# Kernel optimization log

Measured on AMD Instinct MI355X. Metric: run time of the kernel, lower is better.

Reference implementation:

```python
import jax, jax.numpy as jnp
import numpy as np

B, N, D, S, H = 32, 4096, 256, 16, 512
ITERS = 3
EPS = 1e-8
LN_EPS = 1e-5  # torch LayerNorm default


def _ln(x, w, b):
    m = jnp.mean(x, axis=-1, keepdims=True)
    v = jnp.mean(jnp.square(x - m), axis=-1, keepdims=True)
    return (x - m) / jnp.sqrt(v + LN_EPS) * w + b


def setup_inputs() -> dict:
    key = jax.random.key(0)
    ks = jax.random.split(key, 20)
    s = 1.0 / np.sqrt(D)
    return {
        "inputs": jax.random.normal(ks[0], (B, N, D), jnp.float32),
        "token_weight": jax.random.uniform(ks[1], (B, N), jnp.float32),
        "noise": jax.random.normal(ks[2], (B, S, D), jnp.float32),
        "ln_in_w": jnp.ones((D,), jnp.float32), "ln_in_b": jnp.zeros((D,), jnp.float32),
        "ln_s_w": jnp.ones((D,), jnp.float32), "ln_s_b": jnp.zeros((D,), jnp.float32),
        "ln_m_w": jnp.ones((D,), jnp.float32), "ln_m_b": jnp.zeros((D,), jnp.float32),
        "Wk": jax.random.normal(ks[3], (D, D), jnp.float32) * s,
        "Wv": jax.random.normal(ks[4], (D, D), jnp.float32) * s,
        "Wq": jax.random.normal(ks[5], (D, D), jnp.float32) * s,
        "gru_wih": jax.random.normal(ks[6], (3 * D, D), jnp.float32) * s,
        "gru_whh": jax.random.normal(ks[7], (3 * D, D), jnp.float32) * s,
        "gru_bih": jax.random.normal(ks[8], (3 * D,), jnp.float32) * s,
        "gru_bhh": jax.random.normal(ks[9], (3 * D,), jnp.float32) * s,
        "mlp_w1": jax.random.normal(ks[10], (H, D), jnp.float32) * s,
        "mlp_b1": jnp.zeros((H,), jnp.float32),
        "mlp_w2": jax.random.normal(ks[11], (D, H), jnp.float32) * (1.0 / np.sqrt(H)),
        "mlp_b2": jnp.zeros((D,), jnp.float32),
        "slots_mu": jax.random.normal(ks[12], (1, 1, D), jnp.float32) * 0.02,
        "slots_logsigma": jax.random.normal(ks[13], (1, 1, D), jnp.float32) * 0.02,
    }


def _gru(x, h, wih, whh, bih, bhh):
    # torch GRUCell: gates ordered r, z, n
    gi = x @ wih.T + bih  # [BS, 3D]
    gh = h @ whh.T + bhh
    ir, iz, inn = jnp.split(gi, 3, axis=-1)
    hr, hz, hn = jnp.split(gh, 3, axis=-1)
    r = jax.nn.sigmoid(ir + hr)
    z = jax.nn.sigmoid(iz + hz)
    n = jnp.tanh(inn + r * hn)
    return (1.0 - z) * n + z * h


def reference(inputs, token_weight, noise, ln_in_w, ln_in_b, ln_s_w, ln_s_b,
              ln_m_w, ln_m_b, Wk, Wv, Wq, gru_wih, gru_whh, gru_bih, gru_bhh,
              mlp_w1, mlp_b1, mlp_w2, mlp_b2, slots_mu, slots_logsigma):
    tw = jnp.clip(token_weight, 0.0, None)  # [B,N]
    x = _ln(inputs, ln_in_w, ln_in_b)
    k = x @ Wk.T  # [B,N,D]
    v = x @ Wv.T
    sigma = jnp.clip(jnp.exp(slots_logsigma), 1e-6, None)
    slots = slots_mu + sigma * noise  # [B,S,D]
    scale = D ** (-0.5)
    attn = None
    for _ in range(ITERS):
        slots_prev = slots
        q = _ln(slots, ln_s_w, ln_s_b) @ Wq.T  # [B,S,D]
        logits = jnp.einsum('bnd,bmd->bnm', k, q) * scale  # [B,N,S]
        attn = jax.nn.softmax(logits, axis=-1)  # softmax over slots
        attn = attn * tw[:, :, None]
        attn = attn / (jnp.sum(attn, axis=1, keepdims=True) + EPS)  # normalize over tokens
        updates = jnp.einsum('bnm,bnd->bmd', attn, v)  # [B,S,D]
        slots = _gru(updates.reshape(B * S, D), slots_prev.reshape(B * S, D),
                     gru_wih, gru_whh, gru_bih, gru_bhh).reshape(B, S, D)
        h = jax.nn.gelu(_ln(slots, ln_m_w, ln_m_b) @ mlp_w1.T + mlp_b1, approximate=False)
        slots = slots + h @ mlp_w2.T + mlp_b2
    return slots, attn
```

## Files before the change

### kernel.cpp

```cpp
#include <hip/hip_runtime.h>
#include <hip/hip_bf16.h>
#include <math.h>


#define EPS_ 1e-8f
#define LNEPS_ 1e-5f

typedef __attribute__((ext_vector_type(8))) short bf16x8;
typedef __attribute__((ext_vector_type(4))) float f32x4;
typedef __attribute__((ext_vector_type(4))) short s16x4;

static __device__ __forceinline__ short f2bf(float f) {
  __hip_bfloat16 h = __float2bfloat16(f);
  union { __hip_bfloat16 h; short s; } u; u.h = h; return u.s;
}
static __device__ __forceinline__ float4 ld4(const float* p){ return *(const float4*)p; }

__global__ __launch_bounds__(256) void k_prep(
    const float* __restrict__ Wq, const float* __restrict__ Wk,
    const float* __restrict__ wih, const float* __restrict__ Wv,
    const float* __restrict__ whh, const float* __restrict__ w1, const float* __restrict__ w2,
    short* __restrict__ MTb, short* __restrict__ Mb, short* __restrict__ whhb,
    short* __restrict__ w1b, short* __restrict__ w2b) {
  int blk = blockIdx.x, t = threadIdx.x;
  if (blk < 64) {
    int e0 = blk*4;
    float a0=0,a1=0,a2=0,a3=0;
    for (int d=0; d<256; d++) {
      float qv = Wq[d*256 + t];
      a0 += qv*Wk[d*256+e0];   a1 += qv*Wk[d*256+e0+1];
      a2 += qv*Wk[d*256+e0+2]; a3 += qv*Wk[d*256+e0+3];
    }
    MTb[(e0  )*256+t]=f2bf(a0); MTb[(e0+1)*256+t]=f2bf(a1);
    MTb[(e0+2)*256+t]=f2bf(a2); MTb[(e0+3)*256+t]=f2bf(a3);
  } else if (blk < 256) {
    int n0 = (blk-64)*4;
    float a0=0,a1=0,a2=0,a3=0;
    for (int d=0; d<256; d++) {
      float vv = Wv[d*256 + t];
      a0 += wih[(n0  )*256+d]*vv; a1 += wih[(n0+1)*256+d]*vv;
      a2 += wih[(n0+2)*256+d]*vv; a3 += wih[(n0+3)*256+d]*vv;
    }
    Mb[(size_t)(n0  )*256+t]=f2bf(a0); Mb[(size_t)(n0+1)*256+t]=f2bf(a1);
    Mb[(size_t)(n0+2)*256+t]=f2bf(a2); Mb[(size_t)(n0+3)*256+t]=f2bf(a3);
  } else {
    int c = (blk-256)*256 + t;
    const float* src; short* dst;
    if (c < 49152) { src=whh; dst=whhb; }
    else if ((c-=49152) < 32768) { src=w1; dst=w1b; }
    else { c-=32768; src=w2; dst=w2b; }
    float4 v = ld4(src + (size_t)c*4);
    short4 o; o.x=f2bf(v.x); o.y=f2bf(v.y); o.z=f2bf(v.z); o.w=f2bf(v.w);
    *(short4*)(dst + (size_t)c*4) = o;
  }
}

template<int LNIN, int WATTN>
__global__ __launch_bounds__(256) void k3(
    const float* __restrict__ inputs, const float* __restrict__ lnw, const float* __restrict__ lnb,
    short* __restrict__ xbf, const short* __restrict__ qk, const float* __restrict__ twg,
    float* __restrict__ ux_part, float* __restrict__ colsum_part, float* __restrict__ attn_un) {
  __shared__ short Xs[64*264];
  __shared__ short QKs[16*264];
  __shared__ short Pt[16*72];
  __shared__ float tws[64];
  __shared__ float cs[16];
  __shared__ float lnwb[512];
  const int t = threadIdx.x;
  const int b = blockIdx.x >> 4;
  const int n0 = (blockIdx.x & 15) * 256;
  const int lane = t & 63, w = t >> 6, l15 = lane & 15, lg = lane >> 4;
  #pragma unroll
  for (int i=0;i<2;i++){
    int cid = t + i*256;
    int row = cid>>5, ck = cid&31;
    *(uint4*)&QKs[row*264 + ck*8] = *(const uint4*)&qk[((size_t)(b*16+row))*256 + ck*8];
  }
  if (LNIN){
    if (t < 64)       *(float4*)&lnwb[t*4]           = ld4(lnw + t*4);
    else if (t < 128) *(float4*)&lnwb[256+(t-64)*4]  = ld4(lnb + (t-64)*4);
  }
  if (t<16) cs[t]=0.f;
  f32x4 uacc[4] = {};
  for (int g=0; g<4; ++g) {
    __syncthreads();
    const size_t rowbase = (size_t)b*4096 + n0 + g*64;
    if (LNIN) {
      const float* ing = inputs + rowbase*256;
      const int r = t>>2, c = t&3;
      float4 vv[16];
      #pragma unroll
      for (int k=0;k<16;k++) vv[k] = ld4(ing + r*256 + (c+4*k)*4);
      float s=0.f, sq=0.f;
      #pragma unroll
      for (int k=0;k<16;k++){
        s  += vv[k].x+vv[k].y+vv[k].z+vv[k].w;
        sq += vv[k].x*vv[k].x+vv[k].y*vv[k].y+vv[k].z*vv[k].z+vv[k].w*vv[k].w;
      }
      s += __shfl_xor(s,1);  s += __shfl_xor(s,2);
      sq += __shfl_xor(sq,1); sq += __shfl_xor(sq,2);
      float mean = s*(1.f/256.f);
      float rstd = rsqrtf(sq*(1.f/256.f) - mean*mean + LNEPS_);
      short* xw = xbf + rowbase*256;
      #pragma unroll
      for (int k=0;k<16;k++){
        int d0 = (c+4*k)*4;
        float4 wv = *(float4*)&lnwb[d0];
        float4 bv = *(float4*)&lnwb[256+d0];
        s16x4 pk;
        pk[0]=f2bf((vv[k].x-mean)*rstd*wv.x+bv.x);
        pk[1]=f2bf((vv[k].y-mean)*rstd*wv.y+bv.y);
        pk[2]=f2bf((vv[k].z-mean)*rstd*wv.z+bv.z);
        pk[3]=f2bf((vv[k].w-mean)*rstd*wv.w+bv.w);
        *(s16x4*)&Xs[r*264 + d0] = pk;
        *(s16x4*)&xw[r*256 + d0] = pk;
      }
    } else {
      const short* xg = xbf + rowbase*256;
      #pragma unroll
      for (int r8=0;r8<8;r8++){
        int row = r8*8 + (t>>5), ck = t&31;
        *(uint4*)&Xs[row*264 + ck*8] = *(const uint4*)&xg[(size_t)row*256 + ck*8];
      }
    }
    if (t<64) tws[t] = fmaxf(twg[rowbase + t], 0.f);
    __syncthreads();
    f32x4 acc = {0.f,0.f,0.f,0.f};
    #pragma unroll
    for (int kk=0;kk<8;kk++){
      bf16x8 af  = *(const bf16x8*)&Xs[(w*16+l15)*264 + kk*32 + lg*8];
      bf16x8 bfr = *(const bf16x8*)&QKs[l15*264 + kk*32 + lg*8];
      acc = __builtin_amdgcn_mfma_f32_16x16x32_bf16(af, bfr, acc, 0,0,0);
    }
    float a4[4];
    #pragma unroll
    for (int q=0;q<4;q++){
      float v = acc[q]*0.0625f;
      float m = v;
      #pragma unroll
      for (int d=1; d<16; d<<=1) m = fmaxf(m, __shfl_xor(m, d, 16));
      float e = __expf(v-m);
      float se = e;
      #pragma unroll
      for (int d=1; d<16; d<<=1) se += __shfl_xor(se, d, 16);
      int row = w*16 + lg*4 + q;
      float a = (e/se)*tws[row];
      a4[q] = a;
      if (WATTN)
        attn_un[(rowbase + row)*16 + l15] = a;
    }
    float psum = a4[0]+a4[1]+a4[2]+a4[3];
    psum += __shfl_xor(psum, 16);
    psum += __shfl_xor(psum, 32);
    if (lane<16) atomicAdd(&cs[l15], psum);
    s16x4 pk; pk[0]=f2bf(a4[0]); pk[1]=f2bf(a4[1]); pk[2]=f2bf(a4[2]); pk[3]=f2bf(a4[3]);
    *(s16x4*)&Pt[l15*72 + w*16 + lg*4] = pk;
    __syncthreads();
    #pragma unroll
    for (int kk=0;kk<2;kk++){
      bf16x8 a2 = *(const bf16x8*)&Pt[l15*72 + kk*32 + lg*8];
      #pragma unroll
      for (int tt=0;tt<4;tt++){
        int col = w*64 + tt*16 + l15;
        int rbv = kk*32 + lg*8;
        bf16x8 b2;
        #pragma unroll
        for (int j=0;j<8;j++) b2[j] = Xs[(rbv+j)*264 + col];
        uacc[tt] = __builtin_amdgcn_mfma_f32_16x16x32_bf16(a2, b2, uacc[tt], 0,0,0);
      }
    }
  }
  __syncthreads();
  if (t<16) colsum_part[blockIdx.x*16 + t] = cs[t];
  #pragma unroll
  for (int tt=0;tt<4;tt++){
    #pragma unroll
    for (int q=0;q<4;q++)
      ux_part[(size_t)blockIdx.x*4096 + (lg*4+q)*256 + w*64 + tt*16 + l15] = uacc[tt][q];
  }
}

__global__ __launch_bounds__(256) void k_reduce(const float* __restrict__ uxp,
    const float* __restrict__ csp, short* __restrict__ uxr, float* __restrict__ csr) {
  int r = blockIdx.x;
  int b = r>>4, s = r&15;
  int t = threadIdx.x;
  float cs = 0.f;
  #pragma unroll
  for (int k=0;k<16;k++) cs += csp[((b<<4)+k)*16 + s];
  float u = 0.f;
  #pragma unroll
  for (int k=0;k<16;k++) u += uxp[(size_t)((b<<4)+k)*4096 + s*256 + t];
  uxr[(size_t)r*256+t] = f2bf(u/(cs+EPS_));
  if (t==0) csr[r] = cs;
}

__global__ __launch_bounds__(256) void k_gigh(
    const short* __restrict__ uxr, const short* __restrict__ slotsb,
    const short* __restrict__ Mb, const short* __restrict__ whhb,
    const float* __restrict__ bih, const float* __restrict__ bhh,
    float* __restrict__ gig) {
  __shared__ short As[64*40];
  __shared__ short Ws[64*40];
  const int t=threadIdx.x, bn=blockIdx.x, bm=blockIdx.y;
  const short* A; const short* W; const float* bias; int wo;
  if (bn<12) { A=uxr;    W=Mb   + (size_t)bn*64*256;      bias=bih; wo=bn*64; }
  else       { A=slotsb; W=whhb + (size_t)(bn-12)*64*256; bias=bhh; wo=(bn-12)*64; }
  const int w=t>>6, lane=t&63, l15=lane&15, lg=lane>>4;
  f32x4 acc[4]={};
  for (int k0=0;k0<256;k0+=32){
    __syncthreads();
    *(uint4*)&As[(t>>2)*40+(t&3)*8] = *(const uint4*)&A[(size_t)(bm*64+(t>>2))*256 + k0 + (t&3)*8];
    *(uint4*)&Ws[(t>>2)*40+(t&3)*8] = *(const uint4*)&W[(size_t)(t>>2)*256 + k0 + (t&3)*8];
    __syncthreads();
    bf16x8 af = *(const bf16x8*)&As[(w*16+l15)*40+lg*8];
    #pragma unroll
    for (int ct=0;ct<4;ct++){
      bf16x8 bfr = *(const bf16x8*)&Ws[(ct*16+l15)*40+lg*8];
      acc[ct]=__builtin_amdgcn_mfma_f32_16x16x32_bf16(af,bfr,acc[ct],0,0,0);
    }
  }
  #pragma unroll
  for (int ct=0;ct<4;ct++){
    float bv = bias[wo + ct*16 + l15];
    #pragma unroll
    for (int q=0;q<4;q++){
      int row = bm*64 + w*16 + lg*4 + q;
      gig[(size_t)row*1536 + bn*64 + ct*16 + l15] = acc[ct][q] + bv;
    }
  }
}

__global__ __launch_bounds__(256) void k_mlp1(
    const short* __restrict__ lnmb, const short* __restrict__ w1b,
    const float* __restrict__ b1, short* __restrict__ hb) {
  __shared__ short As[64*40];
  __shared__ short Ws[64*40];
  const int t=threadIdx.x, bn=blockIdx.x, bm=blockIdx.y;
  const int w=t>>6, lane=t&63, l15=lane&15, lg=lane>>4;
  f32x4 acc[4]={};
  for (int k0=0;k0<256;k0+=32){
    __syncthreads();
    *(uint4*)&As[(t>>2)*40+(t&3)*8] = *(const uint4*)&lnmb[(size_t)(bm*64+(t>>2))*256 + k0 + (t&3)*8];
    *(uint4*)&Ws[(t>>2)*40+(t&3)*8] = *(const uint4*)&w1b[(size_t)(bn*64+(t>>2))*256 + k0 + (t&3)*8];
    __syncthreads();
    bf16x8 af = *(const bf16x8*)&As[(w*16+l15)*40+lg*8];
    #pragma unroll
    for (int ct=0;ct<4;ct++){
      bf16x8 bfr = *(const bf16x8*)&Ws[(ct*16+l15)*40+lg*8];
      acc[ct]=__builtin_amdgcn_mfma_f32_16x16x32_bf16(af,bfr,acc[ct],0,0,0);
    }
  }
  #pragma unroll
  for (int ct=0;ct<4;ct++){
    float bv = b1[bn*64 + ct*16 + l15];
    #pragma unroll
    for (int q=0;q<4;q++){
      int row = bm*64 + w*16 + lg*4 + q;
      float v = acc[ct][q] + bv;
      v = 0.5f*v*(1.f+erff(v*0.70710678118654752f));
      hb[(size_t)row*512 + bn*64 + ct*16 + l15] = f2bf(v);
    }
  }
}

__global__ __launch_bounds__(256) void k_gates(const float* __restrict__ gig,
    const float* __restrict__ lw, const float* __restrict__ lb,
    float* __restrict__ slots, short* __restrict__ lnmb) {
  int row  = blockIdx.x*4 + (threadIdx.x>>6);
  int lane = threadIdx.x & 63;
  const float* gi = gig + (size_t)row*1536 + lane*4;
  float4 ir = ld4(gi), iz = ld4(gi+256), inn = ld4(gi+512);
  float4 hr = ld4(gi+768), hz = ld4(gi+1024), hn = ld4(gi+1280);
  float* sp = slots + (size_t)row*256 + lane*4;
  float4 h = ld4(sp);
  float hp[4];
  {
    float r0 = 1.f/(1.f+__expf(-(ir.x+hr.x))); float z0 = 1.f/(1.f+__expf(-(iz.x+hz.x)));
    hp[0] = (1.f-z0)*tanhf(inn.x + r0*hn.x) + z0*h.x;
    float r1 = 1.f/(1.f+__expf(-(ir.y+hr.y))); float z1 = 1.f/(1.f+__expf(-(iz.y+hz.y)));
    hp[1] = (1.f-z1)*tanhf(inn.y + r1*hn.y) + z1*h.y;
    float r2 = 1.f/(1.f+__expf(-(ir.z+hr.z))); float z2 = 1.f/(1.f+__expf(-(iz.z+hz.z)));
    hp[2] = (1.f-z2)*tanhf(inn.z + r2*hn.z) + z2*h.z;
    float r3 = 1.f/(1.f+__expf(-(ir.w+hr.w))); float z3 = 1.f/(1.f+__expf(-(iz.w+hz.w)));
    hp[3] = (1.f-z3)*tanhf(inn.w + r3*hn.w) + z3*h.w;
  }
  float s = hp[0]+hp[1]+hp[2]+hp[3];
  float sq = hp[0]*hp[0]+hp[1]*hp[1]+hp[2]*hp[2]+hp[3]*hp[3];
  #pragma unroll
  for (int d=1; d<64; d<<=1) { s += __shfl_xor(s,d); sq += __shfl_xor(sq,d); }
  float mean = s*(1.f/256.f);
  float rstd = rsqrtf(sq*(1.f/256.f) - mean*mean + LNEPS_);
  float4 wv = ld4(lw+lane*4), bv = ld4(lb+lane*4);
  *(float4*)sp = make_float4(hp[0],hp[1],hp[2],hp[3]);
  short4 o;
  o.x = f2bf((hp[0]-mean)*rstd*wv.x+bv.x);
  o.y = f2bf((hp[1]-mean)*rstd*wv.y+bv.y);
  o.z = f2bf((hp[2]-mean)*rstd*wv.z+bv.z);
  o.w = f2bf((hp[3]-mean)*rstd*wv.w+bv.w);
  *(short4*)(lnmb + (size_t)row*256 + lane*4) = o;
}

template<int MODE>
__global__ __launch_bounds__(256) void k_slotend(
    const short* __restrict__ hb, const short* __restrict__ w2b, const float* __restrict__ b2,
    const float* __restrict__ mu, const float* __restrict__ ls, const float* __restrict__ noise,
    const float* __restrict__ res, float* __restrict__ sout, short* __restrict__ slotsb,
    const float* __restrict__ lnsw, const float* __restrict__ lnsb,
    const short* __restrict__ MTb, short* __restrict__ qk) {
  __shared__ short As[64*40];
  __shared__ short Ws[256*40];
  __shared__ short lnS[64*264];
  const int t=threadIdx.x, bm=blockIdx.x;
  const int w=t>>6, lane=t&63, l15=lane&15, lg=lane>>4;
  float v[16][4];
  if (MODE==1) {
    #pragma unroll
    for (int ct=0;ct<16;ct++){
      int col = ct*16+l15;
      float m = mu[col], sg = fmaxf(__expf(ls[col]),1e-6f);
      #pragma unroll
      for (int q=0;q<4;q++){
        int row = bm*64 + w*16 + lg*4 + q;
        v[ct][q] = m + sg*noise[(size_t)row*256+col];
      }
    }
  } else {
    f32x4 acc[16]={};
    for (int k0=0;k0<512;k0+=32){
      __syncthreads();
      *(uint4*)&As[(t>>2)*40+(t&3)*8] = *(const uint4*)&hb[(size_t)(bm*64+(t>>2))*512 + k0 + (t&3)*8];
      #pragma unroll
      for (int i=0;i<4;i++){ int idx=t+i*256;
        *(uint4*)&Ws[(idx>>2)*40+(idx&3)*8] = *(const uint4*)&w2b[(size_t)(idx>>2)*512 + k0 + (idx&3)*8]; }
      __syncthreads();
      bf16x8 af = *(const bf16x8*)&As[(w*16+l15)*40+lg*8];
      #pragma unroll
      for (int ct=0;ct<16;ct++){
        bf16x8 bfr = *(const bf16x8*)&Ws[(ct*16+l15)*40+lg*8];
        acc[ct]=__builtin_amdgcn_mfma_f32_16x16x32_bf16(af,bfr,acc[ct],0,0,0);
      }
    }
    #pragma unroll
    for (int ct=0;ct<16;ct++){
      int col = ct*16+l15;
      float bv = b2[col];
      #pragma unroll
      for (int q=0;q<4;q++){
        int row = bm*64 + w*16 + lg*4 + q;
        v[ct][q] = acc[ct][q] + bv + res[(size_t)row*256+col];
      }
    }
  }
  float s[4]={0,0,0,0}, sq[4]={0,0,0,0};
  #pragma unroll
  for (int ct=0;ct<16;ct++)
    #pragma unroll
    for (int q=0;q<4;q++){ s[q]+=v[ct][q]; sq[q]+=v[ct][q]*v[ct][q]; }
  #pragma unroll
  for (int q=0;q<4;q++){
    #pragma unroll
    for (int d=1; d<16; d<<=1){ s[q]+=__shfl_xor(s[q],d,16); sq[q]+=__shfl_xor(sq[q],d,16); }
  }
  #pragma unroll
  for (int ct=0;ct<16;ct++){
    int col = ct*16+l15;
    float lw = (MODE!=2) ? lnsw[col] : 0.f;
    float lb = (MODE!=2) ? lnsb[col] : 0.f;
    #pragma unroll
    for (int q=0;q<4;q++){
      int row = bm*64 + w*16 + lg*4 + q;
      sout[(size_t)row*256+col] = v[ct][q];
      if (MODE!=2){
        float mean = s[q]*(1.f/256.f);
        float rstd = rsqrtf(sq[q]*(1.f/256.f)-mean*mean+LNEPS_);
        slotsb[(size_t)row*256+col] = f2bf(v[ct][q]);
        lnS[(w*16+lg*4+q)*264 + col] = f2bf((v[ct][q]-mean)*rstd*lw+lb);
      }
    }
  }
  if (MODE!=2){
    f32x4 qa[16]={};
    for (int k0=0;k0<256;k0+=32){
      __syncthreads();
      #pragma unroll
      for (int i=0;i<4;i++){ int idx=t+i*256;
        *(uint4*)&Ws[(idx>>2)*40+(idx&3)*8] = *(const uint4*)&MTb[(size_t)(idx>>2)*256 + k0 + (idx&3)*8]; }
      __syncthreads();
      bf16x8 af = *(const bf16x8*)&lnS[(w*16+l15)*264 + k0 + lg*8];
      #pragma unroll
      for (int ct=0;ct<16;ct++){
        bf16x8 bfr = *(const bf16x8*)&Ws[(ct*16+l15)*40+lg*8];
        qa[ct]=__builtin_amdgcn_mfma_f32_16x16x32_bf16(af,bfr,qa[ct],0,0,0);
      }
    }
    #pragma unroll
    for (int ct=0;ct<16;ct++)
      #pragma unroll
      for (int q=0;q<4;q++)
        qk[(size_t)(bm*64+w*16+lg*4+q)*256 + ct*16+l15] = f2bf(qa[ct][q]);
  }
}

__global__ __launch_bounds__(256) void k_attn_norm(const float* __restrict__ au,
    const float* __restrict__ cs, float* __restrict__ out) {
  size_t i = ((size_t)blockIdx.x*256 + threadIdx.x)*4;
  float4 v = ld4(au + i);
  int s = (int)(i & 15);
  size_t b = i >> 16;
  const float* c = cs + b*16 + s;
  float4 o;
  o.x = v.x/(c[0]+EPS_); o.y = v.y/(c[1]+EPS_);
  o.z = v.z/(c[2]+EPS_); o.w = v.w/(c[3]+EPS_);
  *(float4*)(out + i) = o;
}

extern "C" void kernel_launch(void* const* d_in, const int* in_sizes, int n_in,
                              void* d_out, int out_size, void* d_ws, size_t ws_size,
                              hipStream_t stream) {
  const float* inputs   = (const float*)d_in[0];
  const float* token_w  = (const float*)d_in[1];
  const float* noise    = (const float*)d_in[2];
  const float* ln_in_w  = (const float*)d_in[3];
  const float* ln_in_b  = (const float*)d_in[4];
  const float* ln_s_w   = (const float*)d_in[5];
  const float* ln_s_b   = (const float*)d_in[6];
  const float* ln_m_w   = (const float*)d_in[7];
  const float* ln_m_b   = (const float*)d_in[8];
  const float* Wk       = (const float*)d_in[9];
  const float* Wv       = (const float*)d_in[10];
  const float* Wq       = (const float*)d_in[11];
  const float* gru_wih  = (const float*)d_in[12];
  const float* gru_whh  = (const float*)d_in[13];
  const float* gru_bih  = (const float*)d_in[14];
  const float* gru_bhh  = (const float*)d_in[15];
  const float* mlp_w1   = (const float*)d_in[16];
  const float* mlp_b1   = (const float*)d_in[17];
  const float* mlp_w2   = (const float*)d_in[18];
  const float* mlp_b2   = (const float*)d_in[19];
  const float* slots_mu = (const float*)d_in[20];
  const float* slots_ls = (const float*)d_in[21];

  float* out_slots = (float*)d_out;
  float* out_attn  = out_slots + 131072;

  char* wsb = (char*)d_ws;
  size_t off = 0;
  short* xbf     = (short*)(wsb + off); off += 67108864;
  float* attn_un = (float*)(wsb + off); off += 8388608;
  float* ux_part = (float*)(wsb + off); off += 8388608;
  float* cs_part = (float*)(wsb + off); off += 32768;
  float* cs_red  = (float*)(wsb + off); off += 2048;
  short* qk      = (short*)(wsb + off); off += 262144;
  short* uxr     = (short*)(wsb + off); off += 262144;
  short* MTb     = (short*)(wsb + off); off += 131072;
  short* Mb      = (short*)(wsb + off); off += 393216;
  float* gig     = (float*)(wsb + off); off += 3145728;
  float* slots   = (float*)(wsb + off); off += 524288;
  short* slotsb  = (short*)(wsb + off); off += 262144;
  short* lnmb    = (short*)(wsb + off); off += 262144;
  short* hb      = (short*)(wsb + off); off += 524288;
  short* whhb    = (short*)(wsb + off); off += 393216;
  short* w1b     = (short*)(wsb + off); off += 262144;
  short* w2b     = (short*)(wsb + off); off += 262144;

  k_prep<<<704,256,0,stream>>>(Wq, Wk, gru_wih, Wv, gru_whh, mlp_w1, mlp_w2,
                               MTb, Mb, whhb, w1b, w2b);
  k_slotend<1><<<8,256,0,stream>>>(nullptr, nullptr, nullptr, slots_mu, slots_ls, noise,
                                   nullptr, slots, slotsb, ln_s_w, ln_s_b, MTb, qk);
  for (int it=0; it<3; ++it) {
    if (it==0)
      k3<1,0><<<512,256,0,stream>>>(inputs, ln_in_w, ln_in_b, xbf, qk, token_w,
                                    ux_part, cs_part, attn_un);
    else if (it==1)
      k3<0,0><<<512,256,0,stream>>>(inputs, ln_in_w, ln_in_b, xbf, qk, token_w,
                                    ux_part, cs_part, attn_un);
    else
      k3<0,1><<<512,256,0,stream>>>(inputs, ln_in_w, ln_in_b, xbf, qk, token_w,
                                    ux_part, cs_part, attn_un);
    k_reduce<<<512,256,0,stream>>>(ux_part, cs_part, uxr, cs_red);
    k_gigh<<<dim3(24,8),256,0,stream>>>(uxr, slotsb, Mb, whhb, gru_bih, gru_bhh, gig);
    k_gates<<<128,256,0,stream>>>(gig, ln_m_w, ln_m_b, slots, lnmb);
    k_mlp1<<<dim3(8,8),256,0,stream>>>(lnmb, w1b, mlp_b1, hb);
    if (it<2)
      k_slotend<0><<<8,256,0,stream>>>(hb, w2b, mlp_b2, nullptr, nullptr, nullptr,
                                       slots, slots, slotsb, ln_s_w, ln_s_b, MTb, qk);
    else
      k_slotend<2><<<8,256,0,stream>>>(hb, w2b, mlp_b2, nullptr, nullptr, nullptr,
                                       slots, out_slots, slotsb, ln_s_w, ln_s_b, MTb, qk);
  }
  k_attn_norm<<<2048,256,0,stream>>>(attn_un, cs_red, out_attn);
}
```

Baseline: 241.3 us.

## Fuse per-iteration slot update into one kernel per batch

Replaces the reduce, GRU gate GEMMs, gates/LayerNorm, MLP1, MLP2 and q-projection kernels with a single kernel of 32 blocks (one per batch, 16 slots each) that keeps the intermediates in shared memory. This removes five launches per iteration and the global round trips through gig, hb, lnmb and uxr. The price is low parallelism: only 32 blocks run, and weights are read straight from global memory without LDS staging. The unnormalized attention is now written directly into the output buffer and normalized in place, which drops a scratch buffer.

```diff
diff --git a/kernel.cpp b/kernel.cpp
--- a/kernel.cpp
+++ b/kernel.cpp
@@ -180,230 +180,287 @@
   }
 }
 
-__global__ __launch_bounds__(256) void k_reduce(const float* __restrict__ uxp,
-    const float* __restrict__ csp, short* __restrict__ uxr, float* __restrict__ csr) {
-  int r = blockIdx.x;
-  int b = r>>4, s = r&15;
-  int t = threadIdx.x;
-  float cs = 0.f;
-  #pragma unroll
-  for (int k=0;k<16;k++) cs += csp[((b<<4)+k)*16 + s];
-  float u = 0.f;
-  #pragma unroll
-  for (int k=0;k<16;k++) u += uxp[(size_t)((b<<4)+k)*4096 + s*256 + t];
-  uxr[(size_t)r*256+t] = f2bf(u/(cs+EPS_));
-  if (t==0) csr[r] = cs;
-}
-
-__global__ __launch_bounds__(256) void k_gigh(
-    const short* __restrict__ uxr, const short* __restrict__ slotsb,
+template<int LAST>
+__global__ __launch_bounds__(512) void k_slotiter(
+    const float* __restrict__ uxp, const float* __restrict__ csp,
+    float* __restrict__ csr, float* __restrict__ slots, float* __restrict__ outs,
     const short* __restrict__ Mb, const short* __restrict__ whhb,
     const float* __restrict__ bih, const float* __restrict__ bhh,
-    float* __restrict__ gig) {
-  __shared__ short As[64*40];
-  __shared__ short Ws[64*40];
-  const int t=threadIdx.x, bn=blockIdx.x, bm=blockIdx.y;
-  const short* A; const short* W; const float* bias; int wo;
-  if (bn<12) { A=uxr;    W=Mb   + (size_t)bn*64*256;      bias=bih; wo=bn*64; }
-  else       { A=slotsb; W=whhb + (size_t)(bn-12)*64*256; bias=bhh; wo=(bn-12)*64; }
+    const float* __restrict__ lmw, const float* __restrict__ lmb,
+    const short* __restrict__ w1b, const float* __restrict__ b1,
+    const short* __restrict__ w2b, const float* __restrict__ b2,
+    const float* __restrict__ lsw, const float* __restrict__ lsb,
+    const short* __restrict__ MTb, short* __restrict__ qk)
+{
+  __shared__ short uxA[16*264];
+  __shared__ short slA[16*264];
+  __shared__ float hF [16*260];
+  __shared__ short lnA[16*264];
+  __shared__ short hbA[16*520];
+  __shared__ float csL[16];
+  __shared__ float pS[8][16], pQ[8][16];
+  const int t=threadIdx.x, b=blockIdx.x;
   const int w=t>>6, lane=t&63, l15=lane&15, lg=lane>>4;
-  f32x4 acc[4]={};
-  for (int k0=0;k0<256;k0+=32){
-    __syncthreads();
-    *(uint4*)&As[(t>>2)*40+(t&3)*8] = *(const uint4*)&A[(size_t)(bm*64+(t>>2))*256 + k0 + (t&3)*8];
-    *(uint4*)&Ws[(t>>2)*40+(t&3)*8] = *(const uint4*)&W[(size_t)(t>>2)*256 + k0 + (t&3)*8];
-    __syncthreads();
-    bf16x8 af = *(const bf16x8*)&As[(w*16+l15)*40+lg*8];
+  const int s=t>>5, e=(t&31)*8;
+  if (t<16){
+    float c=0.f;
+    #pragma unroll
+    for (int j=0;j<16;j++) c += csp[((b*16+j)<<4)+t];
+    csL[t]=c+EPS_; csr[b*16+t]=c;
+  }
+  {
+    const float* sp = slots + ((size_t)(b*16+s))*256 + e;
+    float4 v0=ld4(sp), v1=ld4(sp+4);
+    s16x4 o0,o1;
+    o0[0]=f2bf(v0.x);o0[1]=f2bf(v0.y);o0[2]=f2bf(v0.z);o0[3]=f2bf(v0.w);
+    o1[0]=f2bf(v1.x);o1[1]=f2bf(v1.y);o1[2]=f2bf(v1.z);o1[3]=f2bf(v1.w);
+    *(s16x4*)&slA[s*264+e]=o0; *(s16x4*)&slA[s*264+e+4]=o1;
+    *(float4*)&hF[s*260+e]=v0; *(float4*)&hF[s*260+e+4]=v1;
+  }
+  __syncthreads();
+  {
+    float u0=0,u1=0,u2=0,u3=0,u4=0,u5=0,u6=0,u7=0;
+    #pragma unroll
+    for (int j=0;j<16;j++){
+      const float* p = uxp + (((size_t)(b*16+j))<<12) + s*256 + e;
+      float4 a=ld4(p), c=ld4(p+4);
+      u0+=a.x;u1+=a.y;u2+=a.z;u3+=a.w;u4+=c.x;u5+=c.y;u6+=c.z;u7+=c.w;
+    }
+    float inv = 1.f/csL[s];
+    s16x4 o0,o1;
+    o0[0]=f2bf(u0*inv);o0[1]=f2bf(u1*inv);o0[2]=f2bf(u2*inv);o0[3]=f2bf(u3*inv);
+    o1[0]=f2bf(u4*inv);o1[1]=f2bf(u5*inv);o1[2]=f2bf(u6*inv);o1[3]=f2bf(u7*inv);
+    *(s16x4*)&uxA[s*264+e]=o0; *(s16x4*)&uxA[s*264+e+4]=o1;
+  }
+  __syncthreads();
+  f32x4 gh[6], gi[6];
+  #pragma unroll
+  for (int p=0;p<3;p++)
+    #pragma unroll
+    for (int ct=0;ct<2;ct++){
+      int col = p*256 + w*32 + ct*16 + l15;
+      f32x4 ah={},ai={};
+      #pragma unroll
+      for (int kk=0;kk<8;kk++){
+        bf16x8 afs=*(const bf16x8*)&slA[l15*264+kk*32+lg*8];
+        bf16x8 afu=*(const bf16x8*)&uxA[l15*264+kk*32+lg*8];
+        bf16x8 bw=*(const bf16x8*)&whhb[(size_t)col*256+kk*32+lg*8];
+        bf16x8 bm=*(const bf16x8*)&Mb[(size_t)col*256+kk*32+lg*8];
+        ah=__builtin_amdgcn_mfma_f32_16x16x32_bf16(afs,bw,ah,0,0,0);
+        ai=__builtin_amdgcn_mfma_f32_16x16x32_bf16(afu,bm,ai,0,0,0);
+      }
+      gh[p*2+ct]=ah; gi[p*2+ct]=ai;
+    }
+  float hn_[2][4];
+  #pragma unroll
+  for (int ct=0;ct<2;ct++){
+    int c = w*32+ct*16+l15;
+    float bir=bih[c],bhr=bhh[c],biz=bih[256+c],bhz=bhh[256+c],bin=bih[512+c],bhn=bhh[512+c];
+    #pragma unroll
+    for (int q=0;q<4;q++){
+      float r = 1.f/(1.f+__expf(-(gi[ct][q]+bir + gh[ct][q]+bhr)));
+      float z = 1.f/(1.f+__expf(-(gi[2+ct][q]+biz + gh[2+ct][q]+bhz)));
+      float n = tanhf(gi[4+ct][q]+bin + r*(gh[4+ct][q]+bhn));
+      float h = hF[(lg*4+q)*260 + c];
+      hn_[ct][q] = (1.f-z)*n + z*h;
+    }
+  }
+  float s4[4], q4[4];
+  #pragma unroll
+  for (int q=0;q<4;q++){
+    float a=hn_[0][q], c2=hn_[1][q];
+    s4[q]=a+c2; q4[q]=a*a+c2*c2;
+  }
+  #pragma unroll
+  for (int d=1; d<16; d<<=1)
+    #pragma unroll
+    for (int q=0;q<4;q++){ s4[q]+=__shfl_xor(s4[q],d,16); q4[q]+=__shfl_xor(q4[q],d,16); }
+  if (l15==0)
+    #pragma unroll
+    for (int q=0;q<4;q++){ pS[w][lg*4+q]=s4[q]; pQ[w][lg*4+q]=q4[q]; }
+  __syncthreads();
+  float mean_[4], rstd_[4];
+  #pragma unroll
+  for (int q=0;q<4;q++){
+    int row=lg*4+q; float S=0,Q=0;
+    #pragma unroll
+    for (int ww=0;ww<8;ww++){S+=pS[ww][row];Q+=pQ[ww][row];}
+    float m=S*(1.f/256.f); mean_[q]=m; rstd_[q]=rsqrtf(Q*(1.f/256.f)-m*m+LNEPS_);
+  }
+  #pragma unroll
+  for (int ct=0;ct<2;ct++){
+    int c=w*32+ct*16+l15;
+    float lw=lmw[c], lb=lmb[c];
+    #pragma unroll
+    for (int q=0;q<4;q++)
+      lnA[(lg*4+q)*264+c] = f2bf((hn_[ct][q]-mean_[q])*rstd_[q]*lw+lb);
+  }
+  __syncthreads();
+  f32x4 m1[4]={};
+  #pragma unroll
+  for (int kk=0;kk<8;kk++){
+    bf16x8 af=*(const bf16x8*)&lnA[l15*264+kk*32+lg*8];
     #pragma unroll
     for (int ct=0;ct<4;ct++){
-      bf16x8 bfr = *(const bf16x8*)&Ws[(ct*16+l15)*40+lg*8];
-      acc[ct]=__builtin_amdgcn_mfma_f32_16x16x32_bf16(af,bfr,acc[ct],0,0,0);
+      int col=w*64+ct*16+l15;
+      bf16x8 bw=*(const bf16x8*)&w1b[(size_t)col*256+kk*32+lg*8];
+      m1[ct]=__builtin_amdgcn_mfma_f32_16x16x32_bf16(af,bw,m1[ct],0,0,0);
     }
   }
   #pragma unroll
   for (int ct=0;ct<4;ct++){
-    float bv = bias[wo + ct*16 + l15];
+    int col=w*64+ct*16+l15;
+    float bv=b1[col];
     #pragma unroll
     for (int q=0;q<4;q++){
-      int row = bm*64 + w*16 + lg*4 + q;
-      gig[(size_t)row*1536 + bn*64 + ct*16 + l15] = acc[ct][q] + bv;
-    }
-  }
-}
-
-__global__ __launch_bounds__(256) void k_mlp1(
-    const short* __restrict__ lnmb, const short* __restrict__ w1b,
-    const float* __restrict__ b1, short* __restrict__ hb) {
-  __shared__ short As[64*40];
-  __shared__ short Ws[64*40];
-  const int t=threadIdx.x, bn=blockIdx.x, bm=blockIdx.y;
-  const int w=t>>6, lane=t&63, l15=lane&15, lg=lane>>4;
-  f32x4 acc[4]={};
-  for (int k0=0;k0<256;k0+=32){
-    __syncthreads();
-    *(uint4*)&As[(t>>2)*40+(t&3)*8] = *(const uint4*)&lnmb[(size_t)(bm*64+(t>>2))*256 + k0 + (t&3)*8];
-    *(uint4*)&Ws[(t>>2)*40+(t&3)*8] = *(const uint4*)&w1b[(size_t)(bn*64+(t>>2))*256 + k0 + (t&3)*8];
-    __syncthreads();
-    bf16x8 af = *(const bf16x8*)&As[(w*16+l15)*40+lg*8];
-    #pragma unroll
-    for (int ct=0;ct<4;ct++){
-      bf16x8 bfr = *(const bf16x8*)&Ws[(ct*16+l15)*40+lg*8];
-      acc[ct]=__builtin_amdgcn_mfma_f32_16x16x32_bf16(af,bfr,acc[ct],0,0,0);
-    }
-  }
-  #pragma unroll
-  for (int ct=0;ct<4;ct++){
-    float bv = b1[bn*64 + ct*16 + l15];
-    #pragma unroll
-    for (int q=0;q<4;q++){
-      int row = bm*64 + w*16 + lg*4 + q;
-      float v = acc[ct][q] + bv;
-      v = 0.5f*v*(1.f+erff(v*0.70710678118654752f));
-      hb[(size_t)row*512 + bn*64 + ct*16 + l15] = f2bf(v);
-    }
-  }
-}
-
-__global__ __launch_bounds__(256) void k_gates(const float* __restrict__ gig,
-    const float* __restrict__ lw, const float* __restrict__ lb,
-    float* __restrict__ slots, short* __restrict__ lnmb) {
-  int row  = blockIdx.x*4 + (threadIdx.x>>6);
-  int lane = threadIdx.x & 63;
-  const float* gi = gig + (size_t)row*1536 + lane*4;
-  float4 ir = ld4(gi), iz = ld4(gi+256), inn = ld4(gi+512);
-  float4 hr = ld4(gi+768), hz = ld4(gi+1024), hn = ld4(gi+1280);
-  float* sp = slots + (size_t)row*256 + lane*4;
-  float4 h = ld4(sp);
-  float hp[4];
-  {
-    float r0 = 1.f/(1.f+__expf(-(ir.x+hr.x))); float z0 = 1.f/(1.f+__expf(-(iz.x+hz.x)));
-    hp[0] = (1.f-z0)*tanhf(inn.x + r0*hn.x) + z0*h.x;
-    float r1 = 1.f/(1.f+__expf(-(ir.y+hr.y))); float z1 = 1.f/(1.f+__expf(-(iz.y+hz.y)));
-    hp[1] = (1.f-z1)*tanhf(inn.y + r1*hn.y) + z1*h.y;
-    float r2 = 1.f/(1.f+__expf(-(ir.z+hr.z))); float z2 = 1.f/(1.f+__expf(-(iz.z+hz.z)));
-    hp[2] = (1.f-z2)*tanhf(inn.z + r2*hn.z) + z2*h.z;
-    float r3 = 1.f/(1.f+__expf(-(ir.w+hr.w))); float z3 = 1.f/(1.f+__expf(-(iz.w+hz.w)));
-    hp[3] = (1.f-z3)*tanhf(inn.w + r3*hn.w) + z3*h.w;
-  }
-  float s = hp[0]+hp[1]+hp[2]+hp[3];
-  float sq = hp[0]*hp[0]+hp[1]*hp[1]+hp[2]*hp[2]+hp[3]*hp[3];
-  #pragma unroll
-  for (int d=1; d<64; d<<=1) { s += __shfl_xor(s,d); sq += __shfl_xor(sq,d); }
-  float mean = s*(1.f/256.f);
-  float rstd = rsqrtf(sq*(1.f/256.f) - mean*mean + LNEPS_);
-  float4 wv = ld4(lw+lane*4), bv = ld4(lb+lane*4);
-  *(float4*)sp = make_float4(hp[0],hp[1],hp[2],hp[3]);
-  short4 o;
-  o.x = f2bf((hp[0]-mean)*rstd*wv.x+bv.x);
-  o.y = f2bf((hp[1]-mean)*rstd*wv.y+bv.y);
-  o.z = f2bf((hp[2]-mean)*rstd*wv.z+bv.z);
-  o.w = f2bf((hp[3]-mean)*rstd*wv.w+bv.w);
-  *(short4*)(lnmb + (size_t)row*256 + lane*4) = o;
-}
-
-template<int MODE>
-__global__ __launch_bounds__(256) void k_slotend(
-    const short* __restrict__ hb, const short* __restrict__ w2b, const float* __restrict__ b2,
+      float v=m1[ct][q]+bv;
+      v=0.5f*v*(1.f+erff(v*0.70710678118654752f));
+      hbA[(lg*4+q)*520+col]=f2bf(v);
+    }
+  }
+  __syncthreads();
+  f32x4 m2[2]={};
+  #pragma unroll
+  for (int kk=0;kk<16;kk++){
+    bf16x8 af=*(const bf16x8*)&hbA[l15*520+kk*32+lg*8];
+    #pragma unroll
+    for (int ct=0;ct<2;ct++){
+      int col=w*32+ct*16+l15;
+      bf16x8 bw=*(const bf16x8*)&w2b[(size_t)col*512+kk*32+lg*8];
+      m2[ct]=__builtin_amdgcn_mfma_f32_16x16x32_bf16(af,bw,m2[ct],0,0,0);
+    }
+  }
+  float vv[2][4];
+  #pragma unroll
+  for (int ct=0;ct<2;ct++){
+    int col=w*32+ct*16+l15;
+    float bv=b2[col];
+    #pragma unroll
+    for (int q=0;q<4;q++) vv[ct][q]=m2[ct][q]+bv+hn_[ct][q];
+  }
+  float* dst = LAST ? outs : slots;
+  #pragma unroll
+  for (int ct=0;ct<2;ct++){
+    int col=w*32+ct*16+l15;
+    #pragma unroll
+    for (int q=0;q<4;q++)
+      dst[(size_t)(b*16+lg*4+q)*256+col]=vv[ct][q];
+  }
+  if (LAST) return;
+  #pragma unroll
+  for (int q=0;q<4;q++){
+    float a=vv[0][q], c2=vv[1][q];
+    s4[q]=a+c2; q4[q]=a*a+c2*c2;
+  }
+  #pragma unroll
+  for (int d=1; d<16; d<<=1)
+    #pragma unroll
+    for (int q=0;q<4;q++){ s4[q]+=__shfl_xor(s4[q],d,16); q4[q]+=__shfl_xor(q4[q],d,16); }
+  if (l15==0)
+    #pragma unroll
+    for (int q=0;q<4;q++){ pS[w][lg*4+q]=s4[q]; pQ[w][lg*4+q]=q4[q]; }
+  __syncthreads();
+  #pragma unroll
+  for (int q=0;q<4;q++){
+    int row=lg*4+q; float S=0,Q=0;
+    #pragma unroll
+    for (int ww=0;ww<8;ww++){S+=pS[ww][row];Q+=pQ[ww][row];}
+    float m=S*(1.f/256.f); mean_[q]=m; rstd_[q]=rsqrtf(Q*(1.f/256.f)-m*m+LNEPS_);
+  }
+  #pragma unroll
+  for (int ct=0;ct<2;ct++){
+    int c=w*32+ct*16+l15;
+    float lw=lsw[c], lb=lsb[c];
+    #pragma unroll
+    for (int q=0;q<4;q++)
+      lnA[(lg*4+q)*264+c] = f2bf((vv[ct][q]-mean_[q])*rstd_[q]*lw+lb);
+  }
+  __syncthreads();
+  f32x4 qa[2]={};
+  #pragma unroll
+  for (int kk=0;kk<8;kk++){
+    bf16x8 af=*(const bf16x8*)&lnA[l15*264+kk*32+lg*8];
+    #pragma unroll
+    for (int ct=0;ct<2;ct++){
+      int col=w*32+ct*16+l15;
+      bf16x8 bw=*(const bf16x8*)&MTb[(size_t)col*256+kk*32+lg*8];
+      qa[ct]=__builtin_amdgcn_mfma_f32_16x16x32_bf16(af,bw,qa[ct],0,0,0);
+    }
+  }
+  #pragma unroll
+  for (int ct=0;ct<2;ct++){
+    int col=w*32+ct*16+l15;
+    #pragma unroll
+    for (int q=0;q<4;q++)
+      qk[(size_t)(b*16+lg*4+q)*256+col]=f2bf(qa[ct][q]);
+  }
+}
+
+__global__ __launch_bounds__(256) void k_slotinit(
     const float* __restrict__ mu, const float* __restrict__ ls, const float* __restrict__ noise,
-    const float* __restrict__ res, float* __restrict__ sout, short* __restrict__ slotsb,
-    const float* __restrict__ lnsw, const float* __restrict__ lnsb,
+    float* __restrict__ sout, const float* __restrict__ lnsw, const float* __restrict__ lnsb,
     const short* __restrict__ MTb, short* __restrict__ qk) {
-  __shared__ short As[64*40];
   __shared__ short Ws[256*40];
   __shared__ short lnS[64*264];
   const int t=threadIdx.x, bm=blockIdx.x;
   const int w=t>>6, lane=t&63, l15=lane&15, lg=lane>>4;
   float v[16][4];
-  if (MODE==1) {
-    #pragma unroll
-    for (int ct=0;ct<16;ct++){
-      int col = ct*16+l15;
-      float m = mu[col], sg = fmaxf(__expf(ls[col]),1e-6f);
-      #pragma unroll
-      for (int q=0;q<4;q++){
-        int row = bm*64 + w*16 + lg*4 + q;
-        v[ct][q] = m + sg*noise[(size_t)row*256+col];
-      }
-    }
-  } else {
-    f32x4 acc[16]={};
-    for (int k0=0;k0<512;k0+=32){
-      __syncthreads();
-      *(uint4*)&As[(t>>2)*40+(t&3)*8] = *(const uint4*)&hb[(size_t)(bm*64+(t>>2))*512 + k0 + (t&3)*8];
-      #pragma unroll
-      for (int i=0;i<4;i++){ int idx=t+i*256;
-        *(uint4*)&Ws[(idx>>2)*40+(idx&3)*8] = *(const uint4*)&w2b[(size_t)(idx>>2)*512 + k0 + (idx&3)*8]; }
-      __syncthreads();
-      bf16x8 af = *(const bf16x8*)&As[(w*16+l15)*40+lg*8];
-      #pragma unroll
-      for (int ct=0;ct<16;ct++){
-        bf16x8 bfr = *(const bf16x8*)&Ws[(ct*16+l15)*40+lg*8];
-        acc[ct]=__builtin_amdgcn_mfma_f32_16x16x32_bf16(af,bfr,acc[ct],0,0,0);
-      }
-    }
-    #pragma unroll
-    for (int ct=0;ct<16;ct++){
-      int col = ct*16+l15;
-      float bv = b2[col];
-      #pragma unroll
-      for (int q=0;q<4;q++){
-        int row = bm*64 + w*16 + lg*4 + q;
-        v[ct][q] = acc[ct][q] + bv + res[(size_t)row*256+col];
-      }
-    }
-  }
-  float s[4]={0,0,0,0}, sq[4]={0,0,0,0};
-  #pragma unroll
-  for (int ct=0;ct<16;ct++)
-    #pragma unroll
-    for (int q=0;q<4;q++){ s[q]+=v[ct][q]; sq[q]+=v[ct][q]*v[ct][q]; }
-  #pragma unroll
-  for (int q=0;q<4;q++){
-    #pragma unroll
-    for (int d=1; d<16; d<<=1){ s[q]+=__shfl_xor(s[q],d,16); sq[q]+=__shfl_xor(sq[q],d,16); }
-  }
   #pragma unroll
   for (int ct=0;ct<16;ct++){
     int col = ct*16+l15;
-    float lw = (MODE!=2) ? lnsw[col] : 0.f;
-    float lb = (MODE!=2) ? lnsb[col] : 0.f;
+    float m = mu[col], sg = fmaxf(__expf(ls[col]),1e-6f);
+    #pragma unroll
+    for (int q=0;q<4;q++){
+      int row = bm*64 + w*16 + lg*4 + q;
+      v[ct][q] = m + sg*noise[(size_t)row*256+col];
+    }
+  }
+  float s[4]={0,0,0,0}, sq[4]={0,0,0,0};
+  #pragma unroll
+  for (int ct=0;ct<16;ct++)
+    #pragma unroll
+    for (int q=0;q<4;q++){ s[q]+=v[ct][q]; sq[q]+=v[ct][q]*v[ct][q]; }
+  #pragma unroll
+  for (int q=0;q<4;q++){
+    #pragma unroll
+    for (int d=1; d<16; d<<=1){ s[q]+=__shfl_xor(s[q],d,16); sq[q]+=__shfl_xor(sq[q],d,16); }
+  }
+  #pragma unroll
+  for (int ct=0;ct<16;ct++){
+    int col = ct*16+l15;
+    float lw = lnsw[col], lb = lnsb[col];
     #pragma unroll
     for (int q=0;q<4;q++){
       int row = bm*64 + w*16 + lg*4 + q;
       sout[(size_t)row*256+col] = v[ct][q];
-      if (MODE!=2){
-        float mean = s[q]*(1.f/256.f);
-        float rstd = rsqrtf(sq[q]*(1.f/256.f)-mean*mean+LNEPS_);
-        slotsb[(size_t)row*256+col] = f2bf(v[ct][q]);
-        lnS[(w*16+lg*4+q)*264 + col] = f2bf((v[ct][q]-mean)*rstd*lw+lb);
-      }
-    }
-  }
-  if (MODE!=2){
-    f32x4 qa[16]={};
-    for (int k0=0;k0<256;k0+=32){
-      __syncthreads();
-      #pragma unroll
-      for (int i=0;i<4;i++){ int idx=t+i*256;
-        *(uint4*)&Ws[(idx>>2)*40+(idx&3)*8] = *(const uint4*)&MTb[(size_t)(idx>>2)*256 + k0 + (idx&3)*8]; }
-      __syncthreads();
-      bf16x8 af = *(const bf16x8*)&lnS[(w*16+l15)*264 + k0 + lg*8];
-      #pragma unroll
-      for (int ct=0;ct<16;ct++){
-        bf16x8 bfr = *(const bf16x8*)&Ws[(ct*16+l15)*40+lg*8];
-        qa[ct]=__builtin_amdgcn_mfma_f32_16x16x32_bf16(af,bfr,qa[ct],0,0,0);
-      }
-    }
-    #pragma unroll
-    for (int ct=0;ct<16;ct++)
-      #pragma unroll
-      for (int q=0;q<4;q++)
-        qk[(size_t)(bm*64+w*16+lg*4+q)*256 + ct*16+l15] = f2bf(qa[ct][q]);
-  }
-}
-
-__global__ __launch_bounds__(256) void k_attn_norm(const float* __restrict__ au,
-    const float* __restrict__ cs, float* __restrict__ out) {
+      float mean = s[q]*(1.f/256.f);
+      float rstd = rsqrtf(sq[q]*(1.f/256.f)-mean*mean+LNEPS_);
+      lnS[(w*16+lg*4+q)*264 + col] = f2bf((v[ct][q]-mean)*rstd*lw+lb);
+    }
+  }
+  f32x4 qa[16]={};
+  for (int k0=0;k0<256;k0+=32){
+    __syncthreads();
+    #pragma unroll
+    for (int i=0;i<4;i++){ int idx=t+i*256;
+      *(uint4*)&Ws[(idx>>2)*40+(idx&3)*8] = *(const uint4*)&MTb[(size_t)(idx>>2)*256 + k0 + (idx&3)*8]; }
+    __syncthreads();
+    bf16x8 af = *(const bf16x8*)&lnS[(w*16+l15)*264 + k0 + lg*8];
+    #pragma unroll
+    for (int ct=0;ct<16;ct++){
+      bf16x8 bfr = *(const bf16x8*)&Ws[(ct*16+l15)*40+lg*8];
+      qa[ct]=__builtin_amdgcn_mfma_f32_16x16x32_bf16(af,bfr,qa[ct],0,0,0);
+    }
+  }
+  #pragma unroll
+  for (int ct=0;ct<16;ct++)
+    #pragma unroll
+    for (int q=0;q<4;q++)
+      qk[(size_t)(bm*64+w*16+lg*4+q)*256 + ct*16+l15] = f2bf(qa[ct][q]);
+}
+
+__global__ __launch_bounds__(256) void k_attn_norm(float* __restrict__ au,
+    const float* __restrict__ cs) {
   size_t i = ((size_t)blockIdx.x*256 + threadIdx.x)*4;
   float4 v = ld4(au + i);
   int s = (int)(i & 15);
@@ -412,7 +469,7 @@
   float4 o;
   o.x = v.x/(c[0]+EPS_); o.y = v.y/(c[1]+EPS_);
   o.z = v.z/(c[2]+EPS_); o.w = v.w/(c[3]+EPS_);
-  *(float4*)(out + i) = o;
+  *(float4*)(au + i) = o;
 }
 
 extern "C" void kernel_launch(void* const* d_in, const int* in_sizes, int n_in,
@@ -447,47 +504,38 @@
   char* wsb = (char*)d_ws;
   size_t off = 0;
   short* xbf     = (short*)(wsb + off); off += 67108864;
-  float* attn_un = (float*)(wsb + off); off += 8388608;
   float* ux_part = (float*)(wsb + off); off += 8388608;
   float* cs_part = (float*)(wsb + off); off += 32768;
   float* cs_red  = (float*)(wsb + off); off += 2048;
   short* qk      = (short*)(wsb + off); off += 262144;
-  short* uxr     = (short*)(wsb + off); off += 262144;
   short* MTb     = (short*)(wsb + off); off += 131072;
   short* Mb      = (short*)(wsb + off); off += 393216;
-  float* gig     = (float*)(wsb + off); off += 3145728;
   float* slots   = (float*)(wsb + off); off += 524288;
-  short* slotsb  = (short*)(wsb + off); off += 262144;
-  short* lnmb    = (short*)(wsb + off); off += 262144;
-  short* hb      = (short*)(wsb + off); off += 524288;
   short* whhb    = (short*)(wsb + off); off += 393216;
   short* w1b     = (short*)(wsb + off); off += 262144;
   short* w2b     = (short*)(wsb + off); off += 262144;
 
   k_prep<<<704,256,0,stream>>>(Wq, Wk, gru_wih, Wv, gru_whh, mlp_w1, mlp_w2,
                                MTb, Mb, whhb, w1b, w2b);
-  k_slotend<1><<<8,256,0,stream>>>(nullptr, nullptr, nullptr, slots_mu, slots_ls, noise,
-                                   nullptr, slots, slotsb, ln_s_w, ln_s_b, MTb, qk);
+  k_slotinit<<<8,256,0,stream>>>(slots_mu, slots_ls, noise, slots, ln_s_w, ln_s_b, MTb, qk);
   for (int it=0; it<3; ++it) {
     if (it==0)
       k3<1,0><<<512,256,0,stream>>>(inputs, ln_in_w, ln_in_b, xbf, qk, token_w,
-                                    ux_part, cs_part, attn_un);
+                                    ux_part, cs_part, out_attn);
     else if (it==1)
       k3<0,0><<<512,256,0,stream>>>(inputs, ln_in_w, ln_in_b, xbf, qk, token_w,
-                                    ux_part, cs_part, attn_un);
+                                    ux_part, cs_part, out_attn);
     else
       k3<0,1><<<512,256,0,stream>>>(inputs, ln_in_w, ln_in_b, xbf, qk, token_w,
-                                    ux_part, cs_part, attn_un);
-    k_reduce<<<512,256,0,stream>>>(ux_part, cs_part, uxr, cs_red);
-    k_gigh<<<dim3(24,8),256,0,stream>>>(uxr, slotsb, Mb, whhb, gru_bih, gru_bhh, gig);
-    k_gates<<<128,256,0,stream>>>(gig, ln_m_w, ln_m_b, slots, lnmb);
-    k_mlp1<<<dim3(8,8),256,0,stream>>>(lnmb, w1b, mlp_b1, hb);
+                                    ux_part, cs_part, out_attn);
     if (it<2)
-      k_slotend<0><<<8,256,0,stream>>>(hb, w2b, mlp_b2, nullptr, nullptr, nullptr,
-                                       slots, slots, slotsb, ln_s_w, ln_s_b, MTb, qk);
+      k_slotiter<0><<<32,512,0,stream>>>(ux_part, cs_part, cs_red, slots, out_slots,
+                                         Mb, whhb, gru_bih, gru_bhh, ln_m_w, ln_m_b,
+                                         w1b, mlp_b1, w2b, mlp_b2, ln_s_w, ln_s_b, MTb, qk);
     else
-      k_slotend<2><<<8,256,0,stream>>>(hb, w2b, mlp_b2, nullptr, nullptr, nullptr,
-                                       slots, out_slots, slotsb, ln_s_w, ln_s_b, MTb, qk);
-  }
-  k_attn_norm<<<2048,256,0,stream>>>(attn_un, cs_red, out_attn);
-}
+      k_slotiter<1><<<32,512,0,stream>>>(ux_part, cs_part, cs_red, slots, out_slots,
+                                         Mb, whhb, gru_bih, gru_bhh, ln_m_w, ln_m_b,
+                                         w1b, mlp_b1, w2b, mlp_b2, ln_s_w, ln_s_b, MTb, qk);
+  }
+  k_attn_norm<<<2048,256,0,stream>>>(out_attn, cs_red);
+}
```

New measurement: 269.6 us. 11.7% more time.

## Swizzle token tile in LDS, keep q in registers, prefetch next tile

Applied to the files above, without the earlier changes.

Replaces the padded Xs shared-memory layout with an XOR-swizzled unpadded layout, holds the slot-query fragments in registers instead of staging them through shared memory, and software-prefetches the next 64-row bf16 token tile into registers while the current tile is computed. It also writes the unnormalized attention straight into the output buffer and normalizes in place, removing a separate workspace buffer. The aim is fewer LDS bank conflicts, less LDS traffic, and hidden global-load latency in the main attention kernel, at the cost of extra register pressure (8 qk fragments plus 8 prefetch vectors).

```diff
diff --git a/kernel.cpp b/kernel.cpp
--- a/kernel.cpp
+++ b/kernel.cpp
@@ -5,6 +5,7 @@
 
 #define EPS_ 1e-8f
 #define LNEPS_ 1e-5f
+#define XSW(r) ((((r)&7)<<3) ^ ((((r)>>3)&3)<<4))
 
 typedef __attribute__((ext_vector_type(8))) short bf16x8;
 typedef __attribute__((ext_vector_type(4))) float f32x4;
@@ -60,9 +61,8 @@
     const float* __restrict__ inputs, const float* __restrict__ lnw, const float* __restrict__ lnb,
     short* __restrict__ xbf, const short* __restrict__ qk, const float* __restrict__ twg,
     float* __restrict__ ux_part, float* __restrict__ colsum_part, float* __restrict__ attn_un) {
-  __shared__ short Xs[64*264];
-  __shared__ short QKs[16*264];
-  __shared__ short Pt[16*72];
+  __shared__ __align__(16) short Xs[64*256];
+  __shared__ __align__(16) short Pt[16*72];
   __shared__ float tws[64];
   __shared__ float cs[16];
   __shared__ float lnwb[512];
@@ -70,11 +70,11 @@
   const int b = blockIdx.x >> 4;
   const int n0 = (blockIdx.x & 15) * 256;
   const int lane = t & 63, w = t >> 6, l15 = lane & 15, lg = lane >> 4;
-  #pragma unroll
-  for (int i=0;i<2;i++){
-    int cid = t + i*256;
-    int row = cid>>5, ck = cid&31;
-    *(uint4*)&QKs[row*264 + ck*8] = *(const uint4*)&qk[((size_t)(b*16+row))*256 + ck*8];
+  bf16x8 qkf[8];
+  {
+    const short* qrow = qk + ((size_t)(b*16+l15))*256 + lg*8;
+    #pragma unroll
+    for (int kk=0;kk<8;kk++) qkf[kk] = *(const bf16x8*)(qrow + kk*32);
   }
   if (LNIN){
     if (t < 64)       *(float4*)&lnwb[t*4]           = ld4(lnw + t*4);
@@ -82,6 +82,14 @@
   }
   if (t<16) cs[t]=0.f;
   f32x4 uacc[4] = {};
+  const int srow = t>>5, sck = t&31;
+  uint4 pf[8];
+  if (!LNIN){
+    const short* xg = xbf + ((size_t)b*4096 + n0)*256;
+    #pragma unroll
+    for (int r8=0;r8<8;r8++)
+      pf[r8] = *(const uint4*)&xg[(size_t)(r8*8+srow)*256 + sck*8];
+  }
   for (int g=0; g<4; ++g) {
     __syncthreads();
     const size_t rowbase = (size_t)b*4096 + n0 + g*64;
@@ -102,6 +110,7 @@
       float mean = s*(1.f/256.f);
       float rstd = rsqrtf(sq*(1.f/256.f) - mean*mean + LNEPS_);
       short* xw = xbf + rowbase*256;
+      const int sw = XSW(r);
       #pragma unroll
       for (int k=0;k<16;k++){
         int d0 = (c+4*k)*4;
@@ -112,25 +121,32 @@
         pk[1]=f2bf((vv[k].y-mean)*rstd*wv.y+bv.y);
         pk[2]=f2bf((vv[k].z-mean)*rstd*wv.z+bv.z);
         pk[3]=f2bf((vv[k].w-mean)*rstd*wv.w+bv.w);
-        *(s16x4*)&Xs[r*264 + d0] = pk;
+        *(s16x4*)&Xs[r*256 + (d0 ^ sw)] = pk;
         *(s16x4*)&xw[r*256 + d0] = pk;
       }
     } else {
-      const short* xg = xbf + rowbase*256;
       #pragma unroll
       for (int r8=0;r8<8;r8++){
-        int row = r8*8 + (t>>5), ck = t&31;
-        *(uint4*)&Xs[row*264 + ck*8] = *(const uint4*)&xg[(size_t)row*256 + ck*8];
+        int row = r8*8+srow;
+        *(uint4*)&Xs[row*256 + ((sck*8) ^ XSW(row))] = pf[r8];
       }
     }
     if (t<64) tws[t] = fmaxf(twg[rowbase + t], 0.f);
     __syncthreads();
+    if (!LNIN && g<3){
+      const short* xg = xbf + (rowbase+64)*256;
+      #pragma unroll
+      for (int r8=0;r8<8;r8++)
+        pf[r8] = *(const uint4*)&xg[(size_t)(r8*8+srow)*256 + sck*8];
+    }
     f32x4 acc = {0.f,0.f,0.f,0.f};
-    #pragma unroll
-    for (int kk=0;kk<8;kk++){
-      bf16x8 af  = *(const bf16x8*)&Xs[(w*16+l15)*264 + kk*32 + lg*8];
-      bf16x8 bfr = *(const bf16x8*)&QKs[l15*264 + kk*32 + lg*8];
-      acc = __builtin_amdgcn_mfma_f32_16x16x32_bf16(af, bfr, acc, 0,0,0);
+    {
+      const int ra = w*16+l15, sa = XSW(ra);
+      #pragma unroll
+      for (int kk=0;kk<8;kk++){
+        bf16x8 af = *(const bf16x8*)&Xs[ra*256 + ((kk*32+lg*8) ^ sa)];
+        acc = __builtin_amdgcn_mfma_f32_16x16x32_bf16(af, qkf[kk], acc, 0,0,0);
+      }
     }
     float a4[4];
     #pragma unroll
@@ -162,10 +178,12 @@
       #pragma unroll
       for (int tt=0;tt<4;tt++){
         int col = w*64 + tt*16 + l15;
-        int rbv = kk*32 + lg*8;
         bf16x8 b2;
         #pragma unroll
-        for (int j=0;j<8;j++) b2[j] = Xs[(rbv+j)*264 + col];
+        for (int j=0;j<8;j++){
+          int r2 = kk*32 + lg*8 + j;
+          b2[j] = Xs[r2*256 + (col ^ XSW(r2))];
+        }
         uacc[tt] = __builtin_amdgcn_mfma_f32_16x16x32_bf16(a2, b2, uacc[tt], 0,0,0);
       }
     }
@@ -402,8 +420,8 @@
   }
 }
 
-__global__ __launch_bounds__(256) void k_attn_norm(const float* __restrict__ au,
-    const float* __restrict__ cs, float* __restrict__ out) {
+__global__ __launch_bounds__(256) void k_attn_norm(float* __restrict__ au,
+    const float* __restrict__ cs) {
   size_t i = ((size_t)blockIdx.x*256 + threadIdx.x)*4;
   float4 v = ld4(au + i);
   int s = (int)(i & 15);
@@ -412,7 +430,7 @@
   float4 o;
   o.x = v.x/(c[0]+EPS_); o.y = v.y/(c[1]+EPS_);
   o.z = v.z/(c[2]+EPS_); o.w = v.w/(c[3]+EPS_);
-  *(float4*)(out + i) = o;
+  *(float4*)(au + i) = o;
 }
 
 extern "C" void kernel_launch(void* const* d_in, const int* in_sizes, int n_in,
@@ -447,7 +465,6 @@
   char* wsb = (char*)d_ws;
   size_t off = 0;
   short* xbf     = (short*)(wsb + off); off += 67108864;
-  float* attn_un = (float*)(wsb + off); off += 8388608;
   float* ux_part = (float*)(wsb + off); off += 8388608;
   float* cs_part = (float*)(wsb + off); off += 32768;
   float* cs_red  = (float*)(wsb + off); off += 2048;
@@ -471,13 +488,13 @@
   for (int it=0; it<3; ++it) {
     if (it==0)
       k3<1,0><<<512,256,0,stream>>>(inputs, ln_in_w, ln_in_b, xbf, qk, token_w,
-                                    ux_part, cs_part, attn_un);
+                                    ux_part, cs_part, out_attn);
     else if (it==1)
       k3<0,0><<<512,256,0,stream>>>(inputs, ln_in_w, ln_in_b, xbf, qk, token_w,
-                                    ux_part, cs_part, attn_un);
+                                    ux_part, cs_part, out_attn);
     else
       k3<0,1><<<512,256,0,stream>>>(inputs, ln_in_w, ln_in_b, xbf, qk, token_w,
-                                    ux_part, cs_part, attn_un);
+                                    ux_part, cs_part, out_attn);
     k_reduce<<<512,256,0,stream>>>(ux_part, cs_part, uxr, cs_red);
     k_gigh<<<dim3(24,8),256,0,stream>>>(uxr, slotsb, Mb, whhb, gru_bih, gru_bhh, gig);
     k_gates<<<128,256,0,stream>>>(gig, ln_m_w, ln_m_b, slots, lnmb);
@@ -489,5 +506,5 @@
       k_slotend<2><<<8,256,0,stream>>>(hb, w2b, mlp_b2, nullptr, nullptr, nullptr,
                                        slots, out_slots, slotsb, ln_s_w, ln_s_b, MTb, qk);
   }
-  k_attn_norm<<<2048,256,0,stream>>>(attn_un, cs_red, out_attn);
-}
+  k_attn_norm<<<2048,256,0,stream>>>(out_attn, cs_red);
+}
```

New measurement: 273.8 us. 13.5% more time.
